# Performance work log

Measured on AMD Instinct MI355X. Metric: run time of the kernel, lower is better.

## Reference

```python
import jax, jax.numpy as jnp
import numpy as np

B, N, D = 4, 4096, 1024
H, DH = 16, 64            # heads, dim_head; inner = H*DH = 1024
FF = 4 * D                # ffn inner dim
EPS = 1e-5


def setup_inputs() -> dict:
    key = jax.random.key(0)
    ks = jax.random.split(key, 8)
    s = 0.02
    return {
        "x": jax.random.normal(ks[0], (B, N, D), jnp.float32),
        "W_qkv": jax.random.normal(ks[1], (D, 3 * H * DH), jnp.float32) * s,
        "W_out": jax.random.normal(ks[2], (H * DH, D), jnp.float32) * s,
        "b_out": jnp.zeros((D,), jnp.float32),
        "ln_g": jnp.ones((D,), jnp.float32),
        "ln_b": jnp.zeros((D,), jnp.float32),
        "W1": jax.random.normal(ks[3], (D, FF), jnp.float32) * s,
        "b1": jnp.zeros((FF,), jnp.float32),
        "W2": jax.random.normal(ks[4], (FF, D), jnp.float32) * s,
        "b2": jnp.zeros((D,), jnp.float32),
    }


def reference(x, W_qkv, W_out, b_out, ln_g, ln_b, W1, b1, W2, b2):
    b, n, _ = x.shape
    scale = DH ** -0.5

    # --- LinearAttention (dual-softmax kernelized attention) ---
    qkv = x @ W_qkv                                   # [b, n, 3*H*DH]
    q, k, v = jnp.split(qkv, 3, axis=-1)
    split = lambda t: t.reshape(b, n, H, DH).transpose(0, 2, 1, 3)  # [b, h, n, d]
    q = jax.nn.softmax(split(q) * scale, axis=-1)     # softmax over head dim
    k = jax.nn.softmax(split(k), axis=-2)             # softmax over sequence
    v = split(v)
    context = jnp.einsum('bhnd,bhne->bhde', q, k)     # [b, h, d, e] -- linear in n
    out = jnp.einsum('bhde,bhnd->bhne', context, v)   # [b, h, n, e]
    out = out.transpose(0, 2, 1, 3).reshape(b, n, H * DH)
    attn = out @ W_out + b_out                        # to_out (dropout=0 at eval)

    # --- LayerNorm ---
    mu = jnp.mean(attn, axis=-1, keepdims=True)
    var = jnp.var(attn, axis=-1, keepdims=True)
    h = (attn - mu) * jax.lax.rsqrt(var + EPS) * ln_g + ln_b

    # --- FeedForward: Linear -> SiLU -> Linear ---
    y = jax.nn.silu(h @ W1 + b1) @ W2 + b2
    return y
```

## Files before the change

### kernel.cpp

```cpp
#include <hip/hip_runtime.h>
#include <hip/hip_bf16.h>

typedef __bf16 bf16x8 __attribute__((ext_vector_type(8)));
typedef __bf16 bf16x4 __attribute__((ext_vector_type(4)));
typedef float  f32x4  __attribute__((ext_vector_type(4)));

#define GLOAD_LDS16(gp, lp) \
  __builtin_amdgcn_global_load_lds((const __attribute__((address_space(1))) void*)(gp), \
                                   (__attribute__((address_space(3))) void*)(lp), 16, 0, 0)
#define LGKM0 do { asm volatile("s_waitcnt lgkmcnt(0)" ::: "memory"); \
                   __builtin_amdgcn_sched_barrier(0); } while (0)


__global__ __launch_bounds__(256) void zero_f32(float* __restrict__ p, int n) {
  int i = (blockIdx.x * 256 + threadIdx.x) * 4;
  if (i < n) *(float4*)(p + i) = make_float4(0.f, 0.f, 0.f, 0.f);
}

__global__ __launch_bounds__(256) void cvt_f32_bf16(const float* __restrict__ in,
                                                    __bf16* __restrict__ out, long n) {
  long i = ((long)blockIdx.x * 256 + threadIdx.x) * 4;
  if (i >= n) return;
  float4 v = *(const float4*)(in + i);
  bf16x4 o;
  o[0] = (__bf16)v.x; o[1] = (__bf16)v.y; o[2] = (__bf16)v.z; o[3] = (__bf16)v.w;
  *(bf16x4*)(out + i) = o;
}

__global__ __launch_bounds__(256) void cvt_wT(const float* __restrict__ W,
                                              __bf16* __restrict__ WT, int K, int N) {
  __shared__ float t[32][33];
  int k0 = blockIdx.x * 32, n0 = blockIdx.y * 32;
  int tx = threadIdx.x, ty = threadIdx.y;
  #pragma unroll
  for (int i = 0; i < 32; i += 8)
    t[ty + i][tx] = W[(size_t)(k0 + ty + i) * N + n0 + tx];
  __syncthreads();
  #pragma unroll
  for (int i = 0; i < 32; i += 8)
    WT[(size_t)(n0 + ty + i) * K + k0 + tx] = (__bf16)t[tx][ty + i];
}

__global__ __launch_bounds__(256) void prep_all(
    const float* __restrict__ x, __bf16* __restrict__ xb,
    float* __restrict__ Sctx, int nS,
    const float* __restrict__ Wq, __bf16* __restrict__ WqT,
    const float* __restrict__ Wo, __bf16* __restrict__ WoT,
    const float* __restrict__ W1p, __bf16* __restrict__ W1T,
    const float* __restrict__ W2p, __bf16* __restrict__ W2T) {
  const int bid = blockIdx.x, tid = threadIdx.x;
  if (bid < 16384) {
    long i = ((long)bid * 256 + tid) * 4;
    float4 v = *(const float4*)(x + i);
    bf16x4 o;
    o[0] = (__bf16)v.x; o[1] = (__bf16)v.y; o[2] = (__bf16)v.z; o[3] = (__bf16)v.w;
    *(bf16x4*)(xb + i) = o;
    return;
  }
  if (bid < 16644) {
    int i = ((bid - 16384) * 256 + tid) * 4;
    if (i < nS) *(float4*)(Sctx + i) = make_float4(0.f, 0.f, 0.f, 0.f);
    return;
  }
  const float* W; __bf16* WT; int K, N, local, kb, nb;
  if (bid < 19716)      { W = Wq;  WT = WqT; K = 1024; N = 3072; local = bid - 16644; kb = local & 31;  nb = local >> 5; }
  else if (bid < 20740) { W = Wo;  WT = WoT; K = 1024; N = 1024; local = bid - 19716; kb = local & 31;  nb = local >> 5; }
  else if (bid < 24836) { W = W1p; WT = W1T; K = 1024; N = 4096; local = bid - 20740; kb = local & 31;  nb = local >> 5; }
  else                  { W = W2p; WT = W2T; K = 4096; N = 1024; local = bid - 24836; kb = local & 127; nb = local >> 7; }
  __shared__ float t[32][33];
  int k0 = kb * 32, n0 = nb * 32;
  int tx = tid & 31, ty = tid >> 5;
  #pragma unroll
  for (int i = 0; i < 32; i += 8)
    t[ty + i][tx] = W[(size_t)(k0 + ty + i) * N + n0 + tx];
  __syncthreads();
  #pragma unroll
  for (int i = 0; i < 32; i += 8)
    WT[(size_t)(n0 + ty + i) * K + k0 + tx] = (__bf16)t[tx][ty + i];
}


enum { EPI_BF16 = 0, EPI_F32_BIAS = 1, EPI_BF16_SILU = 2, EPI_BF16_BIAS = 3, EPI_QKV = 4 };

template <int EPI>
__global__ __launch_bounds__(512, 1)
void gemm256(const __bf16* __restrict__ A, const __bf16* __restrict__ B,
             void* __restrict__ Cout, const float* __restrict__ bias,
             int M, int N, int K, float* __restrict__ Sq) {
  __shared__ __bf16 lds[65536];
  const int tid = threadIdx.x;
  const int w = tid >> 6, l = tid & 63;
  const int brow = blockIdx.x * 256;
  const int bcol = blockIdx.y * 256;
  const int wr = w >> 2, wc = w & 3;
  const int lr = l & 15;
  const int rdo8 = ((l >> 4) ^ ((lr >> 1) & 3)) << 3;
  const int NT = K >> 6;

  const int aoff = (wr * 128 + lr) * 32 + rdo8;
  const int boff = 16384 + (wc * 64 + lr) * 32 + rdo8;

  const int srow = w * 16 + (l >> 2);
  const int soct8 = ((l & 3) ^ ((l >> 3) & 3)) * 8;
  const __bf16* pA0 = A + (size_t)(brow + srow) * K + soct8;
  const __bf16* pA1 = A + (size_t)(brow + 128 + srow) * K + soct8;
  const __bf16* pB0 = B + (size_t)(bcol + srow) * K + soct8;
  const __bf16* pB1 = B + (size_t)(bcol + 128 + srow) * K + soct8;

  auto stageA = [&](int k, int Tt) {
    size_t cofs = (size_t)Tt * 64 + k * 32;
    __bf16* d = lds + (Tt & 1) * 32768 + k * 8192 + w * 512;
    GLOAD_LDS16(pA0 + cofs, d);
    GLOAD_LDS16(pA1 + cofs, d + 4096);
  };
  auto stageB = [&](int k, int Tt) {
    size_t cofs = (size_t)Tt * 64 + k * 32;
    __bf16* d = lds + (Tt & 1) * 32768 + 16384 + k * 8192 + w * 512;
    GLOAD_LDS16(pB0 + cofs, d);
    GLOAD_LDS16(pB1 + cofs, d + 4096);
  };

  f32x4 acc[8][4] = {};
  bf16x8 afr[4], bfr[4];

  stageA(0, 0); stageB(0, 0);
  stageA(1, 0); stageB(1, 0);
  stageA(0, 1); stageB(0, 1);

  for (int T = 0; T < NT; ++T) {
    const int buf = (T & 1) * 32768;
    const bool s1 = (T + 1 < NT), s2 = (T + 2 < NT);

    if (s1) asm volatile("s_waitcnt vmcnt(8)" ::: "memory");
    else    asm volatile("s_waitcnt vmcnt(4)" ::: "memory");
    __builtin_amdgcn_s_barrier();
    {
      const __bf16* pb = lds + buf + boff;
      const __bf16* pa = lds + buf + aoff;
      #pragma unroll
      for (int n = 0; n < 4; ++n) bfr[n] = *(const bf16x8*)(pb + n * 512);
      #pragma unroll
      for (int m = 0; m < 4; ++m) afr[m] = *(const bf16x8*)(pa + m * 512);
      if (s1) stageA(1, T + 1);
      LGKM0;
      __builtin_amdgcn_s_setprio(1);
      #pragma unroll
      for (int m = 0; m < 4; ++m)
        #pragma unroll
        for (int n = 0; n < 4; ++n)
          acc[m][n] = __builtin_amdgcn_mfma_f32_16x16x32_bf16(afr[m], bfr[n], acc[m][n], 0, 0, 0);
      __builtin_amdgcn_s_setprio(0);
    }

    __builtin_amdgcn_s_barrier();
    {
      const __bf16* pa = lds + buf + aoff + 2048;
      #pragma unroll
      for (int m = 0; m < 4; ++m) afr[m] = *(const bf16x8*)(pa + m * 512);
      if (s1) stageB(1, T + 1);
      LGKM0;
      __builtin_amdgcn_s_setprio(1);
      #pragma unroll
      for (int m = 0; m < 4; ++m)
        #pragma unroll
        for (int n = 0; n < 4; ++n)
          acc[m + 4][n] = __builtin_amdgcn_mfma_f32_16x16x32_bf16(afr[m], bfr[n], acc[m + 4][n], 0, 0, 0);
      __builtin_amdgcn_s_setprio(0);
    }

    if (s1) asm volatile("s_waitcnt vmcnt(8)" ::: "memory");
    else    asm volatile("s_waitcnt vmcnt(0)" ::: "memory");
    __builtin_amdgcn_s_barrier();
    {
      const __bf16* pb = lds + buf + 8192 + boff;
      const __bf16* pa = lds + buf + 8192 + aoff;
      #pragma unroll
      for (int n = 0; n < 4; ++n) bfr[n] = *(const bf16x8*)(pb + n * 512);
      #pragma unroll
      for (int m = 0; m < 4; ++m) afr[m] = *(const bf16x8*)(pa + m * 512);
      if (s2) stageA(0, T + 2);
      LGKM0;
      __builtin_amdgcn_s_setprio(1);
      #pragma unroll
      for (int m = 0; m < 4; ++m)
        #pragma unroll
        for (int n = 0; n < 4; ++n)
          acc[m][n] = __builtin_amdgcn_mfma_f32_16x16x32_bf16(afr[m], bfr[n], acc[m][n], 0, 0, 0);
      __builtin_amdgcn_s_setprio(0);
    }

    __builtin_amdgcn_s_barrier();
    {
      const __bf16* pa = lds + buf + 8192 + aoff + 2048;
      #pragma unroll
      for (int m = 0; m < 4; ++m) afr[m] = *(const bf16x8*)(pa + m * 512);
      if (s2) stageB(0, T + 2);
      LGKM0;
      __builtin_amdgcn_s_setprio(1);
      #pragma unroll
      for (int m = 0; m < 4; ++m)
        #pragma unroll
        for (int n = 0; n < 4; ++n)
          acc[m + 4][n] = __builtin_amdgcn_mfma_f32_16x16x32_bf16(afr[m], bfr[n], acc[m + 4][n], 0, 0, 0);
      __builtin_amdgcn_s_setprio(0);
    }
  }

  if (EPI == EPI_QKV) {
    const int creg = bcol + wc * 64;
    const int region = creg >> 10;
    if (region == 0) {
      #pragma unroll
      for (int m = 0; m < 8; ++m) {
        int row0 = brow + wr * 128 + m * 16 + (l >> 4) * 4;
        #pragma unroll
        for (int j = 0; j < 4; ++j) {
          float v0 = acc[m][0][j] * 0.125f, v1 = acc[m][1][j] * 0.125f;
          float v2 = acc[m][2][j] * 0.125f, v3 = acc[m][3][j] * 0.125f;
          float mx = fmaxf(fmaxf(v0, v1), fmaxf(v2, v3));
          #pragma unroll
          for (int s = 1; s < 16; s <<= 1) mx = fmaxf(mx, __shfl_xor(mx, s));
          float e0 = __expf(v0 - mx), e1 = __expf(v1 - mx);
          float e2 = __expf(v2 - mx), e3 = __expf(v3 - mx);
          float sum = e0 + e1 + e2 + e3;
          #pragma unroll
          for (int s = 1; s < 16; s <<= 1) sum += __shfl_xor(sum, s);
          float inv = 1.f / sum;
          size_t ro = (size_t)(row0 + j) * N + creg + lr;
          ((__bf16*)Cout)[ro]      = (__bf16)(e0 * inv);
          ((__bf16*)Cout)[ro + 16] = (__bf16)(e1 * inv);
          ((__bf16*)Cout)[ro + 32] = (__bf16)(e2 * inv);
          ((__bf16*)Cout)[ro + 48] = (__bf16)(e3 * inv);
        }
      }
    } else if (region == 1) {
      const int batch = brow >> 12;
      float csum[4] = {0.f, 0.f, 0.f, 0.f};
      #pragma unroll
      for (int m = 0; m < 8; ++m) {
        int row0 = brow + wr * 128 + m * 16 + (l >> 4) * 4;
        #pragma unroll
        for (int n = 0; n < 4; ++n) {
          int col = creg + n * 16 + lr;
          #pragma unroll
          for (int j = 0; j < 4; ++j) {
            float e = __expf(acc[m][n][j]);
            __bf16 eb = (__bf16)e;
            ((__bf16*)Cout)[(size_t)(row0 + j) * N + col] = eb;
            csum[n] += (float)eb;
          }
        }
      }
      #pragma unroll
      for (int n = 0; n < 4; ++n) {
        csum[n] += __shfl_xor(csum[n], 16);
        csum[n] += __shfl_xor(csum[n], 32);
      }
      if ((l >> 4) == 0) {
        #pragma unroll
        for (int n = 0; n < 4; ++n)
          atomicAdd(&Sq[batch * 1024 + (creg - 1024) + n * 16 + lr], csum[n]);
      }
    } else {
      #pragma unroll
      for (int m = 0; m < 8; ++m) {
        int row0 = brow + wr * 128 + m * 16 + (l >> 4) * 4;
        #pragma unroll
        for (int n = 0; n < 4; ++n) {
          int col = creg + n * 16 + lr;
          #pragma unroll
          for (int j = 0; j < 4; ++j)
            ((__bf16*)Cout)[(size_t)(row0 + j) * N + col] = (__bf16)acc[m][n][j];
        }
      }
    }
  } else {
    #pragma unroll
    for (int m = 0; m < 8; ++m) {
      int row0 = brow + wr * 128 + m * 16 + (l >> 4) * 4;
      #pragma unroll
      for (int n = 0; n < 4; ++n) {
        int col = bcol + wc * 64 + n * 16 + lr;
        float bv = (EPI == EPI_BF16) ? 0.f : bias[col];
        #pragma unroll
        for (int j = 0; j < 4; ++j) {
          float v = acc[m][n][j];
          size_t off = (size_t)(row0 + j) * N + col;
          if (EPI == EPI_BF16) {
            ((__bf16*)Cout)[off] = (__bf16)v;
          } else if (EPI == EPI_F32_BIAS) {
            ((float*)Cout)[off] = v + bv;
          } else if (EPI == EPI_BF16_BIAS) {
            ((__bf16*)Cout)[off] = (__bf16)(v + bv);
          } else {
            float z = v + bv;
            ((__bf16*)Cout)[off] = (__bf16)(z / (1.f + __expf(-z)));
          }
        }
      }
    }
  }
}


__global__ __launch_bounds__(256) void q_softmax(__bf16* __restrict__ qkv) {
  qkv += (size_t)blockIdx.z * 4096 * 3072;
  int wg = blockIdx.x * 4 + (threadIdx.x >> 6);
  int l = threadIdx.x & 63;
  int row = wg >> 4, h = wg & 15;
  __bf16* p = qkv + (size_t)row * 3072 + h * 64 + l;
  float v = (float)*p * 0.125f;
  float m = v;
  #pragma unroll
  for (int s = 32; s; s >>= 1) m = fmaxf(m, __shfl_xor(m, s));
  float e = __expf(v - m);
  float sum = e;
  #pragma unroll
  for (int s = 32; s; s >>= 1) sum += __shfl_xor(sum, s);
  *p = (__bf16)(e / sum);
}

__global__ __launch_bounds__(256) void k_exp(__bf16* __restrict__ qkv, float* __restrict__ S) {
  qkv += (size_t)blockIdx.z * 4096 * 3072;
  S   += (size_t)blockIdx.z * 1024;
  int c = blockIdx.x * 256 + threadIdx.x;
  int n0 = blockIdx.y * 128;
  float sum = 0.f;
  __bf16* base = qkv + (size_t)n0 * 3072 + 1024 + c;
  for (int i = 0; i < 128; ++i) {
    __bf16* p = base + (size_t)i * 3072;
    float e = __expf((float)*p);
    __bf16 eb = (__bf16)e;
    *p = eb;
    sum += (float)eb;
  }
  atomicAdd(&S[c], sum);
}

__global__ __launch_bounds__(256) void ctx_gemm(const __bf16* __restrict__ qkv,
                                                float* __restrict__ ctx) {
  qkv += (size_t)blockIdx.z * 4096 * 3072;
  ctx += (size_t)blockIdx.z * 16 * 4096;
  int h = blockIdx.x;
  int k0base = blockIdx.y * 1024;
  __shared__ __bf16 sQ[64 * 32];
  __shared__ __bf16 sK[64 * 32];
  int tid = threadIdx.x, w = tid >> 6, l = tid & 63;
  int lr = l & 15, lk = (l >> 4) * 8;
  int srow = tid >> 3, scol = (tid & 7) * 8;
  f32x4 acc[4] = {};

  for (int kc = 0; kc < 1024; kc += 32) {
    size_t grow = (size_t)(k0base + kc + srow) * 3072;
    bf16x8 qv = *(const bf16x8*)(qkv + grow + h * 64 + scol);
    bf16x8 kv = *(const bf16x8*)(qkv + grow + 1024 + h * 64 + scol);
    __syncthreads();
    #pragma unroll
    for (int j = 0; j < 8; ++j) {
      sQ[(scol + j) * 32 + srow] = qv[j];
      sK[(scol + j) * 32 + srow] = kv[j];
    }
    __syncthreads();
    bf16x8 a = *(const bf16x8*)(sQ + (w * 16 + lr) * 32 + lk);
    #pragma unroll
    for (int n = 0; n < 4; ++n) {
      bf16x8 bb = *(const bf16x8*)(sK + (n * 16 + lr) * 32 + lk);
      acc[n] = __builtin_amdgcn_mfma_f32_16x16x32_bf16(a, bb, acc[n], 0, 0, 0);
    }
  }
  float* cbase = ctx + (size_t)h * 64 * 64;
  #pragma unroll
  for (int n = 0; n < 4; ++n) {
    int col = n * 16 + lr;
    #pragma unroll
    for (int j = 0; j < 4; ++j) {
      int row = w * 16 + (l >> 4) * 4 + j;
      atomicAdd(cbase + row * 64 + col, acc[n][j]);
    }
  }
}

__global__ __launch_bounds__(256) void pv_gemm(const __bf16* __restrict__ qkv,
                                               const float* __restrict__ ctx,
                                               const float* __restrict__ S,
                                               __bf16* __restrict__ outpv) {
  qkv   += (size_t)blockIdx.z * 4096 * 3072;
  ctx   += (size_t)blockIdx.z * 16 * 4096;
  S     += (size_t)blockIdx.z * 1024;
  outpv += (size_t)blockIdx.z * 4096 * 1024;
  int h = blockIdx.y;
  int row0 = blockIdx.x * 128;
  __shared__ __bf16 sC[64 * 64];
  int tid = threadIdx.x;
  const float* cb = ctx + (size_t)h * 4096;
  for (int i = tid; i < 4096; i += 256) {
    int d = i >> 6, e = i & 63;
    sC[e * 64 + d] = (__bf16)cb[i];
  }
  __syncthreads();
  int w = tid >> 6, l = tid & 63;
  int lr = l & 15, lk = (l >> 4) * 8;
  f32x4 acc[2][4] = {};
  const __bf16* vbase = qkv + 2048 + h * 64;
  #pragma unroll
  for (int kk = 0; kk < 64; kk += 32) {
    #pragma unroll
    for (int m = 0; m < 2; ++m) {
      int r = row0 + w * 32 + m * 16 + lr;
      bf16x8 a = *(const bf16x8*)(vbase + (size_t)r * 3072 + kk + lk);
      #pragma unroll
      for (int n = 0; n < 4; ++n) {
        bf16x8 bb = *(const bf16x8*)(sC + (n * 16 + lr) * 64 + kk + lk);
        acc[m][n] = __builtin_amdgcn_mfma_f32_16x16x32_bf16(a, bb, acc[m][n], 0, 0, 0);
      }
    }
  }
  #pragma unroll
  for (int m = 0; m < 2; ++m) {
    int rb = row0 + w * 32 + m * 16 + (l >> 4) * 4;
    #pragma unroll
    for (int n = 0; n < 4; ++n) {
      int e = n * 16 + lr;
      float inv = 1.0f / S[h * 64 + e];
      #pragma unroll
      for (int j = 0; j < 4; ++j)
        outpv[(size_t)(rb + j) * 1024 + h * 64 + e] = (__bf16)(acc[m][n][j] * inv);
    }
  }
}

__global__ __launch_bounds__(256) void layernorm_k(const __bf16* __restrict__ attn,
                                                   const float* __restrict__ g,
                                                   const float* __restrict__ beta,
                                                   __bf16* __restrict__ out) {
  int row = blockIdx.x;
  int t = threadIdx.x;
  bf16x4 v4 = *(const bf16x4*)(attn + (size_t)row * 1024 + t * 4);
  float v0 = (float)v4[0], v1 = (float)v4[1], v2 = (float)v4[2], v3 = (float)v4[3];
  float s = v0 + v1 + v2 + v3;
  float ss = v0 * v0 + v1 * v1 + v2 * v2 + v3 * v3;
  #pragma unroll
  for (int sh = 32; sh; sh >>= 1) { s += __shfl_xor(s, sh); ss += __shfl_xor(ss, sh); }
  __shared__ float red[8];
  int w = t >> 6, l = t & 63;
  if (l == 0) { red[w] = s; red[4 + w] = ss; }
  __syncthreads();
  s = red[0] + red[1] + red[2] + red[3];
  ss = red[4] + red[5] + red[6] + red[7];
  float mu = s * (1.f / 1024.f);
  float var = ss * (1.f / 1024.f) - mu * mu;
  float rstd = rsqrtf(var + 1e-5f);
  float4 gg = *(const float4*)(g + t * 4);
  float4 bb = *(const float4*)(beta + t * 4);
  bf16x4 o;
  o[0] = (__bf16)((v0 - mu) * rstd * gg.x + bb.x);
  o[1] = (__bf16)((v1 - mu) * rstd * gg.y + bb.y);
  o[2] = (__bf16)((v2 - mu) * rstd * gg.z + bb.z);
  o[3] = (__bf16)((v3 - mu) * rstd * gg.w + bb.w);
  *(bf16x4*)(out + (size_t)row * 1024 + t * 4) = o;
}


extern "C" void kernel_launch(void* const* d_in, const int* in_sizes, int n_in,
                              void* d_out, int out_size, void* d_ws, size_t ws_size,
                              hipStream_t stream) {
  const float* x     = (const float*)d_in[0];
  const float* W_qkv = (const float*)d_in[1];
  const float* W_out = (const float*)d_in[2];
  const float* b_out = (const float*)d_in[3];
  const float* ln_g  = (const float*)d_in[4];
  const float* ln_b  = (const float*)d_in[5];
  const float* W1    = (const float*)d_in[6];
  const float* b1    = (const float*)d_in[7];
  const float* W2    = (const float*)d_in[8];
  const float* b2    = (const float*)d_in[9];

  char* ws = (char*)d_ws;
  size_t off = 0;
  auto alloc = [&](size_t bytes) { void* p = ws + off; off += (bytes + 255) & ~(size_t)255; return p; };

  __bf16* wqkvT = (__bf16*)alloc(3072ull * 1024 * 2);
  __bf16* woutT = (__bf16*)alloc(1024ull * 1024 * 2);
  __bf16* w1T   = (__bf16*)alloc(4096ull * 1024 * 2);
  __bf16* w2T   = (__bf16*)alloc(1024ull * 4096 * 2);

  const size_t FULL_NEED = 196ull << 20;

  if (ws_size >= FULL_NEED) {
    float*  Sctx  = (float*)alloc((4096ull + 4 * 16 * 4096) * 4);
    __bf16* xb    = (__bf16*)alloc(16384ull * 1024 * 2);
    __bf16* qkv   = (__bf16*)alloc(16384ull * 3072 * 2);
    __bf16* outpv = (__bf16*)alloc(16384ull * 1024 * 2);

    float* S   = Sctx;
    float* ctx = Sctx + 4096;
    __bf16* attn = (__bf16*)((char*)qkv + (64ull << 20));
    __bf16* hln  = xb;
    __bf16* ffn1 = qkv;

    prep_all<<<28932, 256, 0, stream>>>(x, xb, Sctx, 266240,
                                        W_qkv, wqkvT, W_out, woutT, W1, w1T, W2, w2T);

    gemm256<EPI_QKV><<<dim3(64, 12), 512, 0, stream>>>(xb, wqkvT, qkv, nullptr, 16384, 3072, 1024, S);
    ctx_gemm<<<dim3(16, 4, 4), 256, 0, stream>>>(qkv, ctx);
    pv_gemm<<<dim3(32, 16, 4), 256, 0, stream>>>(qkv, ctx, S, outpv);

    gemm256<EPI_BF16_BIAS><<<dim3(64, 4), 512, 0, stream>>>(outpv, woutT, attn, b_out, 16384, 1024, 1024, nullptr);
    layernorm_k<<<16384, 256, 0, stream>>>(attn, ln_g, ln_b, hln);
    gemm256<EPI_BF16_SILU><<<dim3(64, 16), 512, 0, stream>>>(hln, w1T, ffn1, b1, 16384, 4096, 1024, nullptr);
    gemm256<EPI_F32_BIAS><<<dim3(64, 4), 512, 0, stream>>>(ffn1, w2T, (float*)d_out, b2, 16384, 1024, 4096, nullptr);
  } else {
    float*  Sctx  = (float*)alloc(66560ull * 4);
    __bf16* xb    = (__bf16*)alloc(16384ull * 1024 * 2);
    __bf16* outpv = (__bf16*)alloc(16384ull * 1024 * 2);
    __bf16* qkv_b = (__bf16*)alloc(4096ull * 3072 * 2);

    float* S   = Sctx;
    float* ctx = Sctx + 1024;
    __bf16* attn = xb;
    __bf16* hln  = outpv;
    __bf16* fchunk = xb;

    prep_all<<<28932, 256, 0, stream>>>(x, xb, Sctx, 66560,
                                        W_qkv, wqkvT, W_out, woutT, W1, w1T, W2, w2T);

    for (int b = 0; b < 4; ++b) {
      const __bf16* xb_b = xb + (size_t)b * 4096 * 1024;
      gemm256<EPI_BF16><<<dim3(16, 12), 512, 0, stream>>>(xb_b, wqkvT, qkv_b, nullptr, 4096, 3072, 1024, nullptr);
      zero_f32<<<65, 256, 0, stream>>>(Sctx, 66560);
      q_softmax<<<dim3(16384, 1, 1), 256, 0, stream>>>(qkv_b);
      k_exp<<<dim3(4, 32, 1), 256, 0, stream>>>(qkv_b, S);
      ctx_gemm<<<dim3(16, 4, 1), 256, 0, stream>>>(qkv_b, ctx);
      pv_gemm<<<dim3(32, 16, 1), 256, 0, stream>>>(qkv_b, ctx, S, outpv + (size_t)b * 4096 * 1024);
    }

    gemm256<EPI_BF16_BIAS><<<dim3(64, 4), 512, 0, stream>>>(outpv, woutT, attn, b_out, 16384, 1024, 1024, nullptr);
    layernorm_k<<<16384, 256, 0, stream>>>(attn, ln_g, ln_b, hln);

    for (int c = 0; c < 4; ++c) {
      const __bf16* h_c = hln + (size_t)c * 4096 * 1024;
      float* out_c = (float*)d_out + (size_t)c * 4096 * 1024;
      gemm256<EPI_BF16_SILU><<<dim3(16, 16), 512, 0, stream>>>(h_c, w1T, fchunk, b1, 4096, 4096, 1024, nullptr);
      gemm256<EPI_F32_BIAS><<<dim3(16, 4), 512, 0, stream>>>(fchunk, w2T, out_c, b2, 4096, 1024, 4096, nullptr);
    }
  }
}
```

Measured before the change: 527.9 us.

## Use 16-wave 1024-thread GEMM with smaller per-wave tiles and K-step 32

Adds a new GEMM kernel that keeps the 256x256 block tile but runs it with 16 waves instead of 8. Each wave now owns a 64x64 sub-tile, the K step drops to 32, and the pipeline becomes a simpler double buffer using 32K bf16 of LDS. The four large GEMMs in the full-workspace path switch to it, while the old kernel stays for the fallback path. The aim is to hide latency through more waves and lower per-wave register pressure. The cost is twice as many barriers per K and less reuse of fragments within each wave.

```diff
diff --git a/kernel.cpp b/kernel.cpp
--- a/kernel.cpp
+++ b/kernel.cpp
@@ -25,20 +25,6 @@
   bf16x4 o;
   o[0] = (__bf16)v.x; o[1] = (__bf16)v.y; o[2] = (__bf16)v.z; o[3] = (__bf16)v.w;
   *(bf16x4*)(out + i) = o;
-}
-
-__global__ __launch_bounds__(256) void cvt_wT(const float* __restrict__ W,
-                                              __bf16* __restrict__ WT, int K, int N) {
-  __shared__ float t[32][33];
-  int k0 = blockIdx.x * 32, n0 = blockIdx.y * 32;
-  int tx = threadIdx.x, ty = threadIdx.y;
-  #pragma unroll
-  for (int i = 0; i < 32; i += 8)
-    t[ty + i][tx] = W[(size_t)(k0 + ty + i) * N + n0 + tx];
-  __syncthreads();
-  #pragma unroll
-  for (int i = 0; i < 32; i += 8)
-    WT[(size_t)(n0 + ty + i) * K + k0 + tx] = (__bf16)t[tx][ty + i];
 }
 
 __global__ __launch_bounds__(256) void prep_all(
@@ -79,15 +65,15 @@
     WT[(size_t)(n0 + ty + i) * K + k0 + tx] = (__bf16)t[tx][ty + i];
 }
 
-
 enum { EPI_BF16 = 0, EPI_F32_BIAS = 1, EPI_BF16_SILU = 2, EPI_BF16_BIAS = 3, EPI_QKV = 4 };
 
+
 template <int EPI>
-__global__ __launch_bounds__(512, 1)
-void gemm256(const __bf16* __restrict__ A, const __bf16* __restrict__ B,
-             void* __restrict__ Cout, const float* __restrict__ bias,
-             int M, int N, int K, float* __restrict__ Sq) {
-  __shared__ __bf16 lds[65536];
+__global__ __launch_bounds__(1024, 1)
+void gemmW(const __bf16* __restrict__ A, const __bf16* __restrict__ B,
+           void* __restrict__ Cout, const float* __restrict__ bias,
+           int M, int N, int K, float* __restrict__ Sq) {
+  __shared__ __bf16 lds[32768];
   const int tid = threadIdx.x;
   const int w = tid >> 6, l = tid & 63;
   const int brow = blockIdx.x * 256;
@@ -95,115 +81,54 @@
   const int wr = w >> 2, wc = w & 3;
   const int lr = l & 15;
   const int rdo8 = ((l >> 4) ^ ((lr >> 1) & 3)) << 3;
-  const int NT = K >> 6;
-
-  const int aoff = (wr * 128 + lr) * 32 + rdo8;
-  const int boff = 16384 + (wc * 64 + lr) * 32 + rdo8;
-
-  const int srow = w * 16 + (l >> 2);
-  const int soct8 = ((l & 3) ^ ((l >> 3) & 3)) * 8;
-  const __bf16* pA0 = A + (size_t)(brow + srow) * K + soct8;
-  const __bf16* pA1 = A + (size_t)(brow + 128 + srow) * K + soct8;
-  const __bf16* pB0 = B + (size_t)(bcol + srow) * K + soct8;
-  const __bf16* pB1 = B + (size_t)(bcol + 128 + srow) * K + soct8;
-
-  auto stageA = [&](int k, int Tt) {
-    size_t cofs = (size_t)Tt * 64 + k * 32;
-    __bf16* d = lds + (Tt & 1) * 32768 + k * 8192 + w * 512;
-    GLOAD_LDS16(pA0 + cofs, d);
-    GLOAD_LDS16(pA1 + cofs, d + 4096);
+  const int NT = K >> 5;
+
+  const int aoff = (wr * 64 + lr) * 32 + rdo8;
+  const int boff = 8192 + (wc * 64 + lr) * 32 + rdo8;
+
+  const int srow = tid >> 2;
+  const int soct8 = ((tid & 3) ^ ((srow >> 1) & 3)) * 8;
+  const __bf16* pA = A + (size_t)(brow + srow) * K + soct8;
+  const __bf16* pB = B + (size_t)(bcol + srow) * K + soct8;
+  __bf16* const dA = lds + w * 512;
+  __bf16* const dB = lds + 8192 + w * 512;
+
+  f32x4 acc[4][4] = {};
+
+  auto stage = [&](int buf) {
+    GLOAD_LDS16(pA, dA + buf * 16384);
+    GLOAD_LDS16(pB, dB + buf * 16384);
+    pA += 32; pB += 32;
   };
-  auto stageB = [&](int k, int Tt) {
-    size_t cofs = (size_t)Tt * 64 + k * 32;
-    __bf16* d = lds + (Tt & 1) * 32768 + 16384 + k * 8192 + w * 512;
-    GLOAD_LDS16(pB0 + cofs, d);
-    GLOAD_LDS16(pB1 + cofs, d + 4096);
-  };
-
-  f32x4 acc[8][4] = {};
-  bf16x8 afr[4], bfr[4];
-
-  stageA(0, 0); stageB(0, 0);
-  stageA(1, 0); stageB(1, 0);
-  stageA(0, 1); stageB(0, 1);
-
-  for (int T = 0; T < NT; ++T) {
-    const int buf = (T & 1) * 32768;
-    const bool s1 = (T + 1 < NT), s2 = (T + 2 < NT);
-
-    if (s1) asm volatile("s_waitcnt vmcnt(8)" ::: "memory");
-    else    asm volatile("s_waitcnt vmcnt(4)" ::: "memory");
+
+  stage(0); stage(1);
+
+  for (int t = 0; t < NT; ++t) {
+    if (t + 1 < NT) asm volatile("s_waitcnt vmcnt(2)" ::: "memory");
+    else            asm volatile("s_waitcnt vmcnt(0)" ::: "memory");
     __builtin_amdgcn_s_barrier();
-    {
-      const __bf16* pb = lds + buf + boff;
-      const __bf16* pa = lds + buf + aoff;
-      #pragma unroll
-      for (int n = 0; n < 4; ++n) bfr[n] = *(const bf16x8*)(pb + n * 512);
-      #pragma unroll
-      for (int m = 0; m < 4; ++m) afr[m] = *(const bf16x8*)(pa + m * 512);
-      if (s1) stageA(1, T + 1);
-      LGKM0;
-      __builtin_amdgcn_s_setprio(1);
-      #pragma unroll
-      for (int m = 0; m < 4; ++m)
-        #pragma unroll
-        for (int n = 0; n < 4; ++n)
-          acc[m][n] = __builtin_amdgcn_mfma_f32_16x16x32_bf16(afr[m], bfr[n], acc[m][n], 0, 0, 0);
-      __builtin_amdgcn_s_setprio(0);
-    }
-
+
+    const __bf16* sA = lds + (t & 1) * 16384 + aoff;
+    const __bf16* sB = lds + (t & 1) * 16384 + boff;
+    bf16x8 afr[4], bfr[4];
+    #pragma unroll
+    for (int m = 0; m < 4; ++m)
+      afr[m] = *(const bf16x8*)(sA + m * 512);
+    #pragma unroll
+    for (int n = 0; n < 4; ++n)
+      bfr[n] = *(const bf16x8*)(sB + n * 512);
+    LGKM0;
     __builtin_amdgcn_s_barrier();
-    {
-      const __bf16* pa = lds + buf + aoff + 2048;
-      #pragma unroll
-      for (int m = 0; m < 4; ++m) afr[m] = *(const bf16x8*)(pa + m * 512);
-      if (s1) stageB(1, T + 1);
-      LGKM0;
-      __builtin_amdgcn_s_setprio(1);
-      #pragma unroll
-      for (int m = 0; m < 4; ++m)
-        #pragma unroll
-        for (int n = 0; n < 4; ++n)
-          acc[m + 4][n] = __builtin_amdgcn_mfma_f32_16x16x32_bf16(afr[m], bfr[n], acc[m + 4][n], 0, 0, 0);
-      __builtin_amdgcn_s_setprio(0);
-    }
-
-    if (s1) asm volatile("s_waitcnt vmcnt(8)" ::: "memory");
-    else    asm volatile("s_waitcnt vmcnt(0)" ::: "memory");
-    __builtin_amdgcn_s_barrier();
-    {
-      const __bf16* pb = lds + buf + 8192 + boff;
-      const __bf16* pa = lds + buf + 8192 + aoff;
-      #pragma unroll
-      for (int n = 0; n < 4; ++n) bfr[n] = *(const bf16x8*)(pb + n * 512);
-      #pragma unroll
-      for (int m = 0; m < 4; ++m) afr[m] = *(const bf16x8*)(pa + m * 512);
-      if (s2) stageA(0, T + 2);
-      LGKM0;
-      __builtin_amdgcn_s_setprio(1);
-      #pragma unroll
-      for (int m = 0; m < 4; ++m)
-        #pragma unroll
-        for (int n = 0; n < 4; ++n)
-          acc[m][n] = __builtin_amdgcn_mfma_f32_16x16x32_bf16(afr[m], bfr[n], acc[m][n], 0, 0, 0);
-      __builtin_amdgcn_s_setprio(0);
-    }
-
-    __builtin_amdgcn_s_barrier();
-    {
-      const __bf16* pa = lds + buf + 8192 + aoff + 2048;
-      #pragma unroll
-      for (int m = 0; m < 4; ++m) afr[m] = *(const bf16x8*)(pa + m * 512);
-      if (s2) stageB(0, T + 2);
-      LGKM0;
-      __builtin_amdgcn_s_setprio(1);
-      #pragma unroll
-      for (int m = 0; m < 4; ++m)
-        #pragma unroll
-        for (int n = 0; n < 4; ++n)
-          acc[m + 4][n] = __builtin_amdgcn_mfma_f32_16x16x32_bf16(afr[m], bfr[n], acc[m + 4][n], 0, 0, 0);
-      __builtin_amdgcn_s_setprio(0);
-    }
+
+    if (t + 2 < NT) stage(t & 1);
+
+    __builtin_amdgcn_s_setprio(1);
+    #pragma unroll
+    for (int m = 0; m < 4; ++m)
+      #pragma unroll
+      for (int n = 0; n < 4; ++n)
+        acc[m][n] = __builtin_amdgcn_mfma_f32_16x16x32_bf16(afr[m], bfr[n], acc[m][n], 0, 0, 0);
+    __builtin_amdgcn_s_setprio(0);
   }
 
   if (EPI == EPI_QKV) {
@@ -211,8 +136,8 @@
     const int region = creg >> 10;
     if (region == 0) {
       #pragma unroll
-      for (int m = 0; m < 8; ++m) {
-        int row0 = brow + wr * 128 + m * 16 + (l >> 4) * 4;
+      for (int m = 0; m < 4; ++m) {
+        int row0 = brow + wr * 64 + m * 16 + (l >> 4) * 4;
         #pragma unroll
         for (int j = 0; j < 4; ++j) {
           float v0 = acc[m][0][j] * 0.125f, v1 = acc[m][1][j] * 0.125f;
@@ -237,8 +162,8 @@
       const int batch = brow >> 12;
       float csum[4] = {0.f, 0.f, 0.f, 0.f};
       #pragma unroll
-      for (int m = 0; m < 8; ++m) {
-        int row0 = brow + wr * 128 + m * 16 + (l >> 4) * 4;
+      for (int m = 0; m < 4; ++m) {
+        int row0 = brow + wr * 64 + m * 16 + (l >> 4) * 4;
         #pragma unroll
         for (int n = 0; n < 4; ++n) {
           int col = creg + n * 16 + lr;
@@ -263,8 +188,8 @@
       }
     } else {
       #pragma unroll
-      for (int m = 0; m < 8; ++m) {
-        int row0 = brow + wr * 128 + m * 16 + (l >> 4) * 4;
+      for (int m = 0; m < 4; ++m) {
+        int row0 = brow + wr * 64 + m * 16 + (l >> 4) * 4;
         #pragma unroll
         for (int n = 0; n < 4; ++n) {
           int col = creg + n * 16 + lr;
@@ -276,8 +201,8 @@
     }
   } else {
     #pragma unroll
-    for (int m = 0; m < 8; ++m) {
-      int row0 = brow + wr * 128 + m * 16 + (l >> 4) * 4;
+    for (int m = 0; m < 4; ++m) {
+      int row0 = brow + wr * 64 + m * 16 + (l >> 4) * 4;
       #pragma unroll
       for (int n = 0; n < 4; ++n) {
         int col = bcol + wc * 64 + n * 16 + lr;
@@ -296,6 +221,157 @@
             float z = v + bv;
             ((__bf16*)Cout)[off] = (__bf16)(z / (1.f + __expf(-z)));
           }
+        }
+      }
+    }
+  }
+}
+
+
+template <int EPI>
+__global__ __launch_bounds__(512, 1)
+void gemm256(const __bf16* __restrict__ A, const __bf16* __restrict__ B,
+             void* __restrict__ Cout, const float* __restrict__ bias,
+             int M, int N, int K, float* __restrict__ Sq) {
+  __shared__ __bf16 lds[65536];
+  const int tid = threadIdx.x;
+  const int w = tid >> 6, l = tid & 63;
+  const int brow = blockIdx.x * 256;
+  const int bcol = blockIdx.y * 256;
+  const int wr = w >> 2, wc = w & 3;
+  const int lr = l & 15;
+  const int rdo8 = ((l >> 4) ^ ((lr >> 1) & 3)) << 3;
+  const int NT = K >> 6;
+
+  const int aoff = (wr * 128 + lr) * 32 + rdo8;
+  const int boff = 16384 + (wc * 64 + lr) * 32 + rdo8;
+
+  const int srow = w * 16 + (l >> 2);
+  const int soct8 = ((l & 3) ^ ((l >> 3) & 3)) * 8;
+  const __bf16* pA0 = A + (size_t)(brow + srow) * K + soct8;
+  const __bf16* pA1 = A + (size_t)(brow + 128 + srow) * K + soct8;
+  const __bf16* pB0 = B + (size_t)(bcol + srow) * K + soct8;
+  const __bf16* pB1 = B + (size_t)(bcol + 128 + srow) * K + soct8;
+
+  auto stageA = [&](int k, int Tt) {
+    size_t cofs = (size_t)Tt * 64 + k * 32;
+    __bf16* d = lds + (Tt & 1) * 32768 + k * 8192 + w * 512;
+    GLOAD_LDS16(pA0 + cofs, d);
+    GLOAD_LDS16(pA1 + cofs, d + 4096);
+  };
+  auto stageB = [&](int k, int Tt) {
+    size_t cofs = (size_t)Tt * 64 + k * 32;
+    __bf16* d = lds + (Tt & 1) * 32768 + 16384 + k * 8192 + w * 512;
+    GLOAD_LDS16(pB0 + cofs, d);
+    GLOAD_LDS16(pB1 + cofs, d + 4096);
+  };
+
+  f32x4 acc[8][4] = {};
+  bf16x8 afr[4], bfr[4];
+
+  stageA(0, 0); stageB(0, 0);
+  stageA(1, 0); stageB(1, 0);
+  stageA(0, 1); stageB(0, 1);
+
+  for (int T = 0; T < NT; ++T) {
+    const int buf = (T & 1) * 32768;
+    const bool s1 = (T + 1 < NT), s2 = (T + 2 < NT);
+
+    if (s1) asm volatile("s_waitcnt vmcnt(8)" ::: "memory");
+    else    asm volatile("s_waitcnt vmcnt(4)" ::: "memory");
+    __builtin_amdgcn_s_barrier();
+    {
+      const __bf16* pb = lds + buf + boff;
+      const __bf16* pa = lds + buf + aoff;
+      #pragma unroll
+      for (int n = 0; n < 4; ++n) bfr[n] = *(const bf16x8*)(pb + n * 512);
+      #pragma unroll
+      for (int m = 0; m < 4; ++m) afr[m] = *(const bf16x8*)(pa + m * 512);
+      if (s1) stageA(1, T + 1);
+      LGKM0;
+      __builtin_amdgcn_s_setprio(1);
+      #pragma unroll
+      for (int m = 0; m < 4; ++m)
+        #pragma unroll
+        for (int n = 0; n < 4; ++n)
+          acc[m][n] = __builtin_amdgcn_mfma_f32_16x16x32_bf16(afr[m], bfr[n], acc[m][n], 0, 0, 0);
+      __builtin_amdgcn_s_setprio(0);
+    }
+
+    __builtin_amdgcn_s_barrier();
+    {
+      const __bf16* pa = lds + buf + aoff + 2048;
+      #pragma unroll
+      for (int m = 0; m < 4; ++m) afr[m] = *(const bf16x8*)(pa + m * 512);
+      if (s1) stageB(1, T + 1);
+      LGKM0;
+      __builtin_amdgcn_s_setprio(1);
+      #pragma unroll
+      for (int m = 0; m < 4; ++m)
+        #pragma unroll
+        for (int n = 0; n < 4; ++n)
+          acc[m + 4][n] = __builtin_amdgcn_mfma_f32_16x16x32_bf16(afr[m], bfr[n], acc[m + 4][n], 0, 0, 0);
+      __builtin_amdgcn_s_setprio(0);
+    }
+
+    if (s1) asm volatile("s_waitcnt vmcnt(8)" ::: "memory");
+    else    asm volatile("s_waitcnt vmcnt(0)" ::: "memory");
+    __builtin_amdgcn_s_barrier();
+    {
+      const __bf16* pb = lds + buf + 8192 + boff;
+      const __bf16* pa = lds + buf + 8192 + aoff;
+      #pragma unroll
+      for (int n = 0; n < 4; ++n) bfr[n] = *(const bf16x8*)(pb + n * 512);
+      #pragma unroll
+      for (int m = 0; m < 4; ++m) afr[m] = *(const bf16x8*)(pa + m * 512);
+      if (s2) stageA(0, T + 2);
+      LGKM0;
+      __builtin_amdgcn_s_setprio(1);
+      #pragma unroll
+      for (int m = 0; m < 4; ++m)
+        #pragma unroll
+        for (int n = 0; n < 4; ++n)
+          acc[m][n] = __builtin_amdgcn_mfma_f32_16x16x32_bf16(afr[m], bfr[n], acc[m][n], 0, 0, 0);
+      __builtin_amdgcn_s_setprio(0);
+    }
+
+    __builtin_amdgcn_s_barrier();
+    {
+      const __bf16* pa = lds + buf + 8192 + aoff + 2048;
+      #pragma unroll
+      for (int m = 0; m < 4; ++m) afr[m] = *(const bf16x8*)(pa + m * 512);
+      if (s2) stageB(0, T + 2);
+      LGKM0;
+      __builtin_amdgcn_s_setprio(1);
+      #pragma unroll
+      for (int m = 0; m < 4; ++m)
+        #pragma unroll
+        for (int n = 0; n < 4; ++n)
+          acc[m + 4][n] = __builtin_amdgcn_mfma_f32_16x16x32_bf16(afr[m], bfr[n], acc[m + 4][n], 0, 0, 0);
+      __builtin_amdgcn_s_setprio(0);
+    }
+  }
+
+  #pragma unroll
+  for (int m = 0; m < 8; ++m) {
+    int row0 = brow + wr * 128 + m * 16 + (l >> 4) * 4;
+    #pragma unroll
+    for (int n = 0; n < 4; ++n) {
+      int col = bcol + wc * 64 + n * 16 + lr;
+      float bv = (EPI == EPI_BF16) ? 0.f : bias[col];
+      #pragma unroll
+      for (int j = 0; j < 4; ++j) {
+        float v = acc[m][n][j];
+        size_t off = (size_t)(row0 + j) * N + col;
+        if (EPI == EPI_BF16) {
+          ((__bf16*)Cout)[off] = (__bf16)v;
+        } else if (EPI == EPI_F32_BIAS) {
+          ((float*)Cout)[off] = v + bv;
+        } else if (EPI == EPI_BF16_BIAS) {
+          ((__bf16*)Cout)[off] = (__bf16)(v + bv);
+        } else {
+          float z = v + bv;
+          ((__bf16*)Cout)[off] = (__bf16)(z / (1.f + __expf(-z)));
         }
       }
     }
@@ -501,14 +577,14 @@
     prep_all<<<28932, 256, 0, stream>>>(x, xb, Sctx, 266240,
                                         W_qkv, wqkvT, W_out, woutT, W1, w1T, W2, w2T);
 
-    gemm256<EPI_QKV><<<dim3(64, 12), 512, 0, stream>>>(xb, wqkvT, qkv, nullptr, 16384, 3072, 1024, S);
+    gemmW<EPI_QKV><<<dim3(64, 12), 1024, 0, stream>>>(xb, wqkvT, qkv, nullptr, 16384, 3072, 1024, S);
     ctx_gemm<<<dim3(16, 4, 4), 256, 0, stream>>>(qkv, ctx);
     pv_gemm<<<dim3(32, 16, 4), 256, 0, stream>>>(qkv, ctx, S, outpv);
 
-    gemm256<EPI_BF16_BIAS><<<dim3(64, 4), 512, 0, stream>>>(outpv, woutT, attn, b_out, 16384, 1024, 1024, nullptr);
+    gemmW<EPI_BF16_BIAS><<<dim3(64, 4), 1024, 0, stream>>>(outpv, woutT, attn, b_out, 16384, 1024, 1024, nullptr);
     layernorm_k<<<16384, 256, 0, stream>>>(attn, ln_g, ln_b, hln);
-    gemm256<EPI_BF16_SILU><<<dim3(64, 16), 512, 0, stream>>>(hln, w1T, ffn1, b1, 16384, 4096, 1024, nullptr);
-    gemm256<EPI_F32_BIAS><<<dim3(64, 4), 512, 0, stream>>>(ffn1, w2T, (float*)d_out, b2, 16384, 1024, 4096, nullptr);
+    gemmW<EPI_BF16_SILU><<<dim3(64, 16), 1024, 0, stream>>>(hln, w1T, ffn1, b1, 16384, 4096, 1024, nullptr);
+    gemmW<EPI_F32_BIAS><<<dim3(64, 4), 1024, 0, stream>>>(ffn1, w2T, (float*)d_out, b2, 16384, 1024, 4096, nullptr);
   } else {
     float*  Sctx  = (float*)alloc(66560ull * 4);
     __bf16* xb    = (__bf16*)alloc(16384ull * 1024 * 2);
```

After: 536.5 us. Within noise of the previous version (+1.6%).
